# Optimization experiments

Measured on AMD Instinct MI355X. Metric: run time of the kernel, lower is better.

## Reference

```python
import jax, jax.numpy as jnp
import numpy as np

FM = 128       # feature_maps
QM = 128       # query_maps
ROUNDS = 4     # test_rounds (training=False)
N_VARS = 24576
N_CLAUSES = 98304
N_EDGES = 3 * N_CLAUSES
EPS = 1e-6


def _dense(k, fan_in, fan_out):
    return jax.random.normal(k, (fan_in, fan_out), jnp.float32) * (1.0 / np.sqrt(fan_in))


def setup_inputs() -> dict:
    key = jax.random.key(0)
    ks = jax.random.split(key, 20)
    return {
        "edge_lit": jax.random.randint(ks[0], (N_EDGES,), 0, 2 * N_VARS, dtype=jnp.int32),
        "edge_clause": jnp.sort(jax.random.randint(ks[1], (N_EDGES,), 0, N_CLAUSES, dtype=jnp.int32)),
        "noise_v": jax.random.normal(ks[2], (ROUNDS, N_VARS, 4), jnp.float32),
        "noise_c": jax.random.normal(ks[3], (ROUNDS, N_CLAUSES, 4), jnp.float32),
        # variables_query: MLP(2, QM, QM), input FM+4
        "vq_w0": _dense(ks[4], FM + 4, QM), "vq_b0": jnp.zeros((QM,), jnp.float32),
        "vq_w1": _dense(ks[5], QM, QM),     "vq_b1": jnp.zeros((QM,), jnp.float32),
        # clauses_query: MLP(2, QM, QM), input FM+4
        "cq_w0": _dense(ks[6], FM + 4, QM), "cq_b0": jnp.zeros((QM,), jnp.float32),
        "cq_w1": _dense(ks[7], QM, QM),     "cq_b1": jnp.zeros((QM,), jnp.float32),
        # clause_update: MLP(2, 2*FM, FM+QM), input FM+2*QM=384
        "cm_w0": _dense(ks[8], FM + 2 * QM, 2 * FM), "cm_b0": jnp.zeros((2 * FM,), jnp.float32),
        "cm_w1": _dense(ks[9], 2 * FM, FM + QM),     "cm_b1": jnp.zeros((FM + QM,), jnp.float32),
        # update_gate: MLP(3, 2*FM, FM), input QM+FM+2*QM=512
        "ug_w0": _dense(ks[10], QM + FM + 2 * QM, 2 * FM), "ug_b0": jnp.zeros((2 * FM,), jnp.float32),
        "ug_w1": _dense(ks[11], 2 * FM, 2 * FM),           "ug_b1": jnp.zeros((2 * FM,), jnp.float32),
        "ug_w2": _dense(ks[12], 2 * FM, FM),               "ug_b2": jnp.zeros((FM,), jnp.float32),
        # clauses_mask_output: MLP(2, FM, 1)
        "co_w0": _dense(ks[13], FM, FM), "co_b0": jnp.zeros((FM,), jnp.float32),
        "co_w1": _dense(ks[14], FM, 1),  "co_b1": jnp.zeros((1,), jnp.float32),
        "n_vars": N_VARS,
        "n_clauses": N_CLAUSES,
    }


def _forward(edge_lit, edge_clause, n_vars, n_clauses, floats):
    (noise_v, noise_c,
     vq_w0, vq_b0, vq_w1, vq_b1,
     cq_w0, cq_b0, cq_w1, cq_b1,
     cm_w0, cm_b0, cm_w1, cm_b1,
     ug_w0, ug_b0, ug_w1, ug_b1, ug_w2, ug_b2,
     co_w0, co_b0, co_w1, co_b1) = floats

    n_edges = edge_lit.shape[0]
    # lit_degree = row sums of sparse adjacency (all nonzeros are 1.0)
    lit_degree = jax.ops.segment_sum(jnp.ones((n_edges,), jnp.float32), edge_lit,
                                     num_segments=2 * n_vars)[:, None]          # [2V,1]
    degree_weight = jax.lax.rsqrt(jnp.maximum(lit_degree, 1.0))
    var_degree_weight = 4.0 * jax.lax.rsqrt(
        jnp.maximum(lit_degree[:n_vars] + lit_degree[n_vars:], 1.0))            # [V,1]

    def mlp2(x, w0, b0, w1, b1):
        return jax.nn.relu(x @ w0 + b0) @ w1 + b1

    def mlp3(x, w0, b0, w1, b1, w2, b2):
        h = jax.nn.relu(x @ w0 + b0)
        h = jax.nn.relu(h @ w1 + b1)
        return h @ w2 + b2

    def pair_norm(x):
        # PairNorm(subtract_mean=True), single graph -> global mean over nodes
        x = x - jnp.mean(x, axis=0, keepdims=True)
        return x * jax.lax.rsqrt(jnp.mean(jnp.square(x)) + EPS)

    def clauses_loss_fn(vq, cq):
        # unsat_cnf_clauses_loss: softplus literal values aggregated per clause,
        # clause satisfiability exp(-sum), gated by clause query mask.
        lits = jax.nn.softplus(jnp.concatenate([vq, -vq], axis=0))              # [2V,Q]
        csum = jax.ops.segment_sum(lits[edge_lit], edge_clause,
                                   num_segments=n_clauses)                      # [C,Q]
        loss = jnp.exp(-csum) * jax.nn.sigmoid(cq)
        return jnp.mean(loss), loss

    grad_fn = jax.grad(clauses_loss_fn, argnums=(0, 1), has_aux=True)

    def step(carry, xs):
        variables, clauses = carry
        nv, nc = xs
        vq = mlp2(jnp.concatenate([variables, nv], -1), vq_w0, vq_b0, vq_w1, vq_b1)
        cq = mlp2(jnp.concatenate([clauses, nc], -1), cq_w0, cq_b0, cq_w1, cq_b1)
        (vgrad, cgrad), clauses_loss = grad_fn(vq, cq)
        vgrad = vgrad * var_degree_weight
        clauses_loss = clauses_loss * 4.0
        clause_data = mlp2(jnp.concatenate([clauses, clauses_loss, cgrad], -1),
                           cm_w0, cm_b0, cm_w1, cm_b1)                          # [C,FM+QM]
        variables_loss_all = clause_data[:, :QM]
        clauses = pair_norm(clause_data[:, QM:]) * 0.25 + 0.1 * clauses
        # adj_matrix @ variables_loss_all (literal-side aggregation)
        variables_loss = jax.ops.segment_sum(variables_loss_all[edge_clause], edge_lit,
                                             num_segments=2 * n_vars) * degree_weight
        unit = jnp.concatenate([vgrad, variables,
                                variables_loss[:n_vars], variables_loss[n_vars:]], -1)
        variables = pair_norm(mlp3(unit, ug_w0, ug_b0, ug_w1, ug_b1, ug_w2, ug_b2)) * 0.25 \
                    + 0.1 * variables
        logits = mlp2(clauses, co_w0, co_b0, co_w1, co_b1)[:, 0]                # [C]
        return (variables, clauses), logits

    init = (jnp.ones((n_vars, FM), jnp.float32), jnp.ones((n_clauses, FM), jnp.float32))
    _, logits = jax.lax.scan(step, init, (noise_v, noise_c))                    # [R,C]
    return jax.nn.sigmoid(logits), jax.nn.softplus(logits)


def reference(edge_lit, edge_clause, noise_v, noise_c,
              vq_w0, vq_b0, vq_w1, vq_b1,
              cq_w0, cq_b0, cq_w1, cq_b1,
              cm_w0, cm_b0, cm_w1, cm_b1,
              ug_w0, ug_b0, ug_w1, ug_b1, ug_w2, ug_b2,
              co_w0, co_b0, co_w1, co_b1,
              n_vars, n_clauses):
    floats = (noise_v, noise_c,
              vq_w0, vq_b0, vq_w1, vq_b1,
              cq_w0, cq_b0, cq_w1, cq_b1,
              cm_w0, cm_b0, cm_w1, cm_b1,
              ug_w0, ug_b0, ug_w1, ug_b1, ug_w2, ug_b2,
              co_w0, co_b0, co_w1, co_b1)
    return _forward(edge_lit, edge_clause, int(n_vars), int(n_clauses), floats)
```

## Files before the change

### kernel.cpp

```cpp
#include <hip/hip_runtime.h>
#include <math.h>

#define NV 24576
#define NC 98304
#define NE 294912
#define CMCHUNK 24576

typedef unsigned short bf16;
typedef _Float16 f16;
using bf8 = __attribute__((ext_vector_type(8))) short;
using f4  = __attribute__((ext_vector_type(4))) float;

static constexpr float INV_CQM = 1.0f / 12582912.0f;
static constexpr float LOG2E = 1.44269504f;
static constexpr float LN2 = 0.69314718f;

__device__ __forceinline__ float b2f(bf16 h) { return __uint_as_float(((unsigned)h) << 16); }
__device__ __forceinline__ bf16 f2b(float f) {
  unsigned u = __float_as_uint(f);
  u += 0x7fff + ((u >> 16) & 1);
  return (bf16)(u >> 16);
}
__device__ __forceinline__ float fexp2(float x) { float r; asm("v_exp_f32 %0, %1" : "=v"(r) : "v"(x)); return r; }
__device__ __forceinline__ float flog2(float x) { float r; asm("v_log_f32 %0, %1" : "=v"(r) : "v"(x)); return r; }
__device__ __forceinline__ float frcpf(float x) { float r; asm("v_rcp_f32 %0, %1" : "=v"(r) : "v"(x)); return r; }
__device__ __forceinline__ float fsigm(float x) { return frcpf(1.0f + fexp2(-x * LOG2E)); }
__device__ __forceinline__ float fsoftplus(float x) {
  return fmaxf(x, 0.0f) + LN2 * flog2(1.0f + fexp2(-fabsf(x) * LOG2E));
}
__device__ __forceinline__ float cvt_ld(float x) { return x; }
__device__ __forceinline__ float cvt_ld(bf16 x) { return b2f(x); }

__device__ __forceinline__ void gload16(const void* g, void* l) {
  __builtin_amdgcn_global_load_lds((const __attribute__((address_space(1))) unsigned int*)g,
                                   (__attribute__((address_space(3))) unsigned int*)l, 16, 0, 0);
}


__global__ __launch_bounds__(256) void k_cptr(const int* __restrict__ ec, int* __restrict__ ptr) {
  int c = blockIdx.x * 256 + threadIdx.x;
  if (c > NC) return;
  int lo = 0, hi = NE;
  while (lo < hi) { int mid = (lo + hi) >> 1; if (ec[mid] < c) lo = mid + 1; else hi = mid; }
  ptr[c] = lo;
}

__global__ __launch_bounds__(256) void k_litcnt(const int* __restrict__ el, int* __restrict__ cnt) {
  int e = blockIdx.x * 256 + threadIdx.x;
  atomicAdd(&cnt[el[e]], 1);
}

__global__ __launch_bounds__(1024) void k_scan(int* __restrict__ cnt, int* __restrict__ ptr) {
  __shared__ int wsum[16];
  __shared__ int carry_s;
  int tid = threadIdx.x, lane = tid & 63, w = tid >> 6;
  if (tid == 0) carry_s = 0;
  __syncthreads();
  for (int base = 0; base < 2 * NV; base += 1024) {
    int x = cnt[base + tid];
    int v = x;
#pragma unroll
    for (int off = 1; off < 64; off <<= 1) {
      int y = __shfl_up(v, off, 64);
      if (lane >= off) v += y;
    }
    if (lane == 63) wsum[w] = v;
    __syncthreads();
    int carry = carry_s;
    int wpre = 0;
    for (int i = 0; i < w; ++i) wpre += wsum[i];
    int excl = carry + wpre + (v - x);
    ptr[base + tid] = excl;
    cnt[base + tid] = excl;
    __syncthreads();
    if (tid == 1023) carry_s = carry + wpre + v;
  }
  __syncthreads();
  if (tid == 0) ptr[2 * NV] = carry_s;
}

__global__ __launch_bounds__(256) void k_fillsort(const int* __restrict__ el, const int* __restrict__ ec,
                                                  int* __restrict__ cur, int* __restrict__ lclause) {
  int e = blockIdx.x * 256 + threadIdx.x;
  int pos = atomicAdd(&cur[el[e]], 1);
  lclause[pos] = ec[e];
}

__global__ __launch_bounds__(256) void k_degree(const int* __restrict__ lptr, float* __restrict__ dw,
                                                float* __restrict__ vdw) {
  int l = blockIdx.x * 256 + threadIdx.x;
  if (l < 2 * NV) dw[l] = rsqrtf(fmaxf((float)(lptr[l + 1] - lptr[l]), 1.0f));
  if (l < NV) {
    int d = (lptr[l + 1] - lptr[l]) + (lptr[l + NV + 1] - lptr[l + NV]);
    vdw[l] = 4.0f * rsqrtf(fmaxf((float)d, 1.0f));
  }
}

__global__ __launch_bounds__(256) void k_init_v(float* __restrict__ variables, bf16* __restrict__ ugA) {
  int i = blockIdx.x * 256 + threadIdx.x;
  variables[i] = 1.0f;
  ugA[(size_t)(i >> 7) * 512 + 128 + (i & 127)] = 0x3F80;
}
__global__ __launch_bounds__(256) void k_init_c(bf16* __restrict__ cmA) {
  int i = blockIdx.x * 256 + threadIdx.x;
  cmA[(size_t)(i >> 7) * 384 + (i & 127)] = 0x3F80;
}

__global__ __launch_bounds__(256) void k_wt(const float* __restrict__ w, bf16* __restrict__ wt,
                                            int K, int N, int Kpad) {
  int idx = blockIdx.x * 256 + threadIdx.x;
  int n = idx / Kpad, k = idx % Kpad;
  if (n >= N) return;
  wt[idx] = (k < K) ? f2b(w[(size_t)k * N + n]) : (bf16)0;
}


template <int KDIM, bool CONCAT, bool RELU, int OUT>
__global__ __launch_bounds__(256) void mgemm(const bf16* __restrict__ A0, int lda,
                                             const float* __restrict__ noise,
                                             const bf16* __restrict__ WT,
                                             const float* __restrict__ Bv,
                                             void* out0, void* out1, int ldOut) {
  __shared__ __align__(16) char smem[65536];
  constexpr int NT = KDIM / 64;
  const int tid = threadIdx.x;
  const int m0 = blockIdx.x * 128;
  const int n0 = blockIdx.y * 128;
  const int lane = tid & 63;
  const int w = tid >> 6;
  const int wr = w >> 1, wc = w & 1;
  const int rl = (tid >> 3) & 7;
  const int cc = tid & 7;
  const int swzoff = (cc * 16) ^ (rl << 4);

  auto stage = [&](int t, int buf) {
    char* As = smem + buf * 32768;
    char* Bs = As + 16384;
    const int k0 = t * 64;
    if (!CONCAT || k0 < 128) {
#pragma unroll
      for (int it = 0; it < 4; ++it) {
        int row0 = it * 32 + w * 8;
        int row = row0 + rl;
        gload16((const char*)(A0 + (size_t)(m0 + row) * lda + k0) + swzoff, As + row0 * 128);
        gload16((const char*)(WT + (size_t)(n0 + row) * KDIM + k0) + swzoff, Bs + row0 * 128);
      }
    } else {
      const int srow = tid >> 3, schunk = tid & 7;
#pragma unroll
      for (int it = 0; it < 4; ++it) {
        int row = srow + it * 32;
        alignas(16) bf16 tmp[8];
#pragma unroll
        for (int e = 0; e < 8; ++e) {
          int kk = schunk * 8 + e;
          tmp[e] = (kk < 4) ? f2b(noise[(size_t)(m0 + row) * 4 + kk]) : (bf16)0;
        }
        *reinterpret_cast<uint4*>(&As[row * 128 + ((schunk * 16) ^ ((row & 7) << 4))]) =
            *reinterpret_cast<uint4*>(tmp);
        int row0 = it * 32 + w * 8;
        gload16((const char*)(WT + (size_t)(n0 + row0 + rl) * KDIM + k0) + swzoff, Bs + row0 * 128);
      }
    }
  };

  f4 acc[4][4] = {};
  stage(0, 0);
#pragma unroll
  for (int t = 0; t < NT; ++t) {
    const int buf = t & 1;
    __builtin_amdgcn_sched_barrier(0);
    if (t + 1 < NT) {
      stage(t + 1, buf ^ 1);
      if (CONCAT && (t + 1) * 64 >= 128) {
        asm volatile("s_waitcnt vmcnt(4) lgkmcnt(0)" ::: "memory");
      } else {
        asm volatile("s_waitcnt vmcnt(8) lgkmcnt(0)" ::: "memory");
      }
    } else {
      asm volatile("s_waitcnt vmcnt(0) lgkmcnt(0)" ::: "memory");
    }
    __builtin_amdgcn_s_barrier();
    __builtin_amdgcn_sched_barrier(0);
    const char* As = smem + buf * 32768;
    const char* Bs = As + 16384;
#pragma unroll
    for (int kk = 0; kk < 2; ++kk) {
      bf8 a[4], b[4];
#pragma unroll
      for (int i = 0; i < 4; ++i) {
        int r = wr * 64 + i * 16 + (lane & 15);
        int cby = (kk * 64 + ((lane >> 4) * 16)) ^ ((r & 7) << 4);
        a[i] = *reinterpret_cast<const bf8*>(&As[r * 128 + cby]);
        int c = wc * 64 + i * 16 + (lane & 15);
        int cby2 = (kk * 64 + ((lane >> 4) * 16)) ^ ((c & 7) << 4);
        b[i] = *reinterpret_cast<const bf8*>(&Bs[c * 128 + cby2]);
      }
#pragma unroll
      for (int i = 0; i < 4; ++i)
#pragma unroll
        for (int j = 0; j < 4; ++j)
          acc[i][j] = __builtin_amdgcn_mfma_f32_16x16x32_bf16(a[i], b[j], acc[i][j], 0, 0, 0);
    }
    __builtin_amdgcn_sched_barrier(0);
    __builtin_amdgcn_s_barrier();
  }
  const int colloc = wc * 64 + (lane & 15);
  const int rowbase = m0 + wr * 64 + ((lane >> 4) << 2);

  if constexpr (OUT == 4) {
    const float* w1 = (const float*)out1;
    float* outp = (float*)out0;
    const int t = ldOut;
    float part[4][4];
#pragma unroll
    for (int i = 0; i < 4; ++i)
#pragma unroll
      for (int p = 0; p < 4; ++p) part[i][p] = 0.0f;
#pragma unroll
    for (int j = 0; j < 4; ++j) {
      int c = colloc + j * 16;
      float bias = Bv[c];
      float w1c = w1[c];
#pragma unroll
      for (int i = 0; i < 4; ++i)
#pragma unroll
        for (int p = 0; p < 4; ++p)
          part[i][p] += fmaxf(acc[i][j][p] + bias, 0.0f) * w1c;
    }
#pragma unroll
    for (int m = 1; m < 16; m <<= 1)
#pragma unroll
      for (int i = 0; i < 4; ++i)
#pragma unroll
        for (int p = 0; p < 4; ++p)
          part[i][p] += __shfl_xor(part[i][p], m, 64);
    float* red = (float*)smem;
    if ((lane & 15) == 0) {
#pragma unroll
      for (int i = 0; i < 4; ++i)
#pragma unroll
        for (int p = 0; p < 4; ++p)
          red[wc * 128 + wr * 64 + i * 16 + ((lane >> 4) << 2) + p] = part[i][p];
    }
    __syncthreads();
    if (tid < 128) {
      float lg = red[tid] + red[128 + tid] + noise[0];
      int row = m0 + tid;
      outp[(size_t)t * NC + row] = fsigm(lg);
      outp[(size_t)4 * NC + (size_t)t * NC + row] = fsoftplus(lg);
    }
    return;
  }

#pragma unroll
  for (int j = 0; j < 4; ++j) {
    int c = n0 + colloc + j * 16;
    float bias = Bv[c];
#pragma unroll
    for (int i = 0; i < 4; ++i) {
      int rb = rowbase + i * 16;
#pragma unroll
      for (int p = 0; p < 4; ++p) {
        float v = acc[i][j][p] + bias;
        if (RELU) v = fmaxf(v, 0.0f);
        int r = rb + p;
        if constexpr (OUT == 0) {
          ((float*)out0)[(size_t)r * ldOut + c] = v;
        } else if constexpr (OUT == 1) {
          ((bf16*)out0)[(size_t)r * ldOut + c] = f2b(v);
        } else if constexpr (OUT == 2) {
          bf16* o = (c < 128) ? (bf16*)out0 : (bf16*)out1;
          o[(size_t)r * 128 + (c & 127)] = f2b(v);
        } else {
          float tq = LN2 * flog2(1.0f + fexp2(-fabsf(v) * LOG2E));
          ((f16*)out0)[(size_t)r * 128 + c] = (f16)(fmaxf(v, 0.0f) + tq);
          ((f16*)out1)[(size_t)r * 128 + c] = (f16)(fmaxf(-v, 0.0f) + tq);
        }
      }
    }
  }
}


__global__ __launch_bounds__(256) void k_loss(const int* __restrict__ edge_lit, const int* __restrict__ cptr,
                                              const f16* __restrict__ sp, const bf16* __restrict__ cq,
                                              bf16* __restrict__ cmA) {
  const int g = threadIdx.x >> 7;
  const int q = threadIdx.x & 127;
  const int c0 = blockIdx.x * 16 + g * 8;
#pragma unroll
  for (int ci = 0; ci < 8; ++ci) {
    int c = c0 + ci;
    int e0 = cptr[c], e1 = cptr[c + 1];
    float csum = 0.0f;
    for (int e = e0; e < e1; e += 4) {
#pragma unroll
      for (int k = 0; k < 4; ++k) {
        int ee = e + k;
        bool ok = ee < e1;
        int lit = ok ? edge_lit[ee] : 0;
        float v = ok ? (float)sp[(size_t)lit * 128 + q] : 0.0f;
        csum += v;
      }
    }
    float s = fsigm(b2f(cq[(size_t)c * 128 + q]));
    float L = fexp2(-csum * LOG2E) * s;
    cmA[(size_t)c * 384 + 128 + q] = f2b(4.0f * L);
    cmA[(size_t)c * 384 + 256 + q] = f2b(L * (1.0f - s) * INV_CQM);
  }
}

__global__ __launch_bounds__(256) void k_gatherv(const int* __restrict__ lptr, const int* __restrict__ lclause,
                                                 const bf16* __restrict__ cmA, const bf16* __restrict__ cd0,
                                                 const f16* __restrict__ spn, const float* __restrict__ dw,
                                                 const float* __restrict__ vdw, bf16* __restrict__ ugA) {
  int v = blockIdx.x;
  int half = threadIdx.x >> 7, q = threadIdx.x & 127;
  int l = v + half * NV;
  int j0 = lptr[l], j1 = lptr[l + 1];
  float sg = 0.0f, sv = 0.0f;
  for (int j = j0; j < j1; j += 4) {
#pragma unroll
    for (int k = 0; k < 4; ++k) {
      int jj = j + k;
      bool ok = jj < j1;
      int c = ok ? lclause[jj] : 0;
      float a = ok ? b2f(cmA[(size_t)c * 384 + 128 + q]) : 0.0f;
      float b = ok ? b2f(cd0[(size_t)c * 128 + q]) : 0.0f;
      sg += a;
      sv += b;
    }
  }
  __shared__ float sgl[2][128];
  sgl[half][q] = sg;
  ugA[(size_t)v * 512 + 256 + half * 128 + q] = f2b(sv * dw[l]);
  __syncthreads();
  if (half == 0) {
    float s = fexp2(-LOG2E * (float)spn[(size_t)v * 128 + q]);
    float g = ((1.0f - s) * sgl[1][q] - s * sgl[0][q]) * (INV_CQM * 0.25f) * vdw[v];
    ugA[(size_t)v * 512 + q] = f2b(g);
  }
}

template <typename T>
__global__ __launch_bounds__(256) void k_pn_stats(const T* __restrict__ X, int R, float* __restrict__ stats) {
  int q = threadIdx.x & 127;
  int rg = threadIdx.x >> 7;
  float cs = 0.0f, ss = 0.0f;
  for (int r = blockIdx.x * 2 + rg; r < R; r += gridDim.x * 2) {
    float x = cvt_ld(X[(size_t)r * 128 + q]);
    cs += x;
    ss += x * x;
  }
  __shared__ float scs[256], sss[256];
  scs[threadIdx.x] = cs;
  sss[threadIdx.x] = ss;
  __syncthreads();
  if (threadIdx.x < 128) atomicAdd(&stats[q], scs[q] + scs[128 + q]);
  for (int off = 128; off; off >>= 1) {
    if (threadIdx.x < off) sss[threadIdx.x] += sss[threadIdx.x + off];
    __syncthreads();
  }
  if (threadIdx.x == 0) atomicAdd(&stats[128], sss[0]);
}

__global__ __launch_bounds__(128) void k_pn_final(float* __restrict__ stats, float R) {
  __shared__ float s[128];
  int q = threadIdx.x;
  float m = stats[q] / R;
  s[q] = m * m;
  __syncthreads();
  for (int off = 64; off; off >>= 1) {
    if (q < off) s[q] += s[q + off];
    __syncthreads();
  }
  if (q == 0) {
    float var = (stats[128] - R * s[0]) / (R * 128.0f);
    stats[129] = rsqrtf(fmaxf(var, 0.0f) + 1e-6f) * 0.25f;
  }
  stats[q] = m;
}

__global__ __launch_bounds__(256) void k_pn_apply_c(const bf16* __restrict__ cd1, const float* __restrict__ stats,
                                                    bf16* __restrict__ cmA) {
  int i = blockIdx.x * 256 + threadIdx.x;
  int c = i >> 7, q = i & 127;
  float x = b2f(cd1[i]);
  float old = b2f(cmA[(size_t)c * 384 + q]);
  cmA[(size_t)c * 384 + q] = f2b((x - stats[q]) * stats[129] + 0.1f * old);
}

__global__ __launch_bounds__(256) void k_pn_apply_v(const float* __restrict__ uout, const float* __restrict__ stats,
                                                    float* __restrict__ variables, bf16* __restrict__ ugA) {
  int i = blockIdx.x * 256 + threadIdx.x;
  int v = i >> 7, q = i & 127;
  float nv = (uout[i] - stats[q]) * stats[129] + 0.1f * variables[i];
  variables[i] = nv;
  ugA[(size_t)v * 512 + 128 + q] = f2b(nv);
}


extern "C" void kernel_launch(void* const* d_in, const int* in_sizes, int n_in,
                              void* d_out, int out_size, void* d_ws, size_t ws_size,
                              hipStream_t stream) {
  const int* edge_lit = (const int*)d_in[0];
  const int* edge_clause = (const int*)d_in[1];
  const float* noise_v = (const float*)d_in[2];
  const float* noise_c = (const float*)d_in[3];
  const float* vq_w0 = (const float*)d_in[4];  const float* vq_b0 = (const float*)d_in[5];
  const float* vq_w1 = (const float*)d_in[6];  const float* vq_b1 = (const float*)d_in[7];
  const float* cq_w0 = (const float*)d_in[8];  const float* cq_b0 = (const float*)d_in[9];
  const float* cq_w1 = (const float*)d_in[10]; const float* cq_b1 = (const float*)d_in[11];
  const float* cm_w0 = (const float*)d_in[12]; const float* cm_b0 = (const float*)d_in[13];
  const float* cm_w1 = (const float*)d_in[14]; const float* cm_b1 = (const float*)d_in[15];
  const float* ug_w0 = (const float*)d_in[16]; const float* ug_b0 = (const float*)d_in[17];
  const float* ug_w1 = (const float*)d_in[18]; const float* ug_b1 = (const float*)d_in[19];
  const float* ug_w2 = (const float*)d_in[20]; const float* ug_b2 = (const float*)d_in[21];
  const float* co_w0 = (const float*)d_in[22]; const float* co_b0 = (const float*)d_in[23];
  const float* co_w1 = (const float*)d_in[24]; const float* co_b1 = (const float*)d_in[25];
  float* out = (float*)d_out;

  char* base = (char*)d_ws;
  size_t off = 0;
  auto A = [&](size_t n) -> char* {
    char* p = base + off;
    off = (off + n + 255) & ~(size_t)255;
    return p;
  };
  float* variables = (float*)A((size_t)NV * 128 * 4);
  bf16* cmA        = (bf16*)A((size_t)NC * 384 * 2);
  bf16* ugA        = (bf16*)A((size_t)NV * 512 * 2);
  char* R_cq       = A((size_t)NC * 128 * 2);
  char* R_h        = A((size_t)NC * 128 * 2);
  char* R_big      = A((size_t)2 * NV * 128 * 2 + (size_t)NV * 128 * 4);
  bf16* wtb        = (bf16*)A(983424);
  int* cptr = (int*)A((size_t)(NC + 1) * 4);
  int* lptr = (int*)A((size_t)(2 * NV + 1) * 4);
  int* lcur = (int*)A((size_t)2 * NV * 4);
  int* lclause = (int*)A((size_t)NE * 4);
  float* dw  = (float*)A((size_t)2 * NV * 4);
  float* vdw = (float*)A((size_t)NV * 4);
  float* stats = (float*)A(2048);
  if (off > ws_size) {
    hipMemsetAsync(d_out, 0xFF, (size_t)out_size * 4, stream);
    return;
  }

  bf16* cq  = (bf16*)R_cq;
  bf16* cd0 = (bf16*)R_cq;
  bf16* hv  = (bf16*)R_h;
  bf16* hc  = (bf16*)R_h;
  bf16* cd1 = (bf16*)R_h;
  bf16* uh1 = (bf16*)R_h;
  bf16* uh2 = (bf16*)(R_h + (size_t)NV * 256 * 2);
  bf16* cmh = (bf16*)R_big;
  f16* spp  = (f16*)(R_big + 12582912);
  f16* spn  = spp + (size_t)NV * 128;
  float* uout = (float*)(R_big + 12582912);

  size_t wo = 0;
  auto WTa = [&](int n, int kp) { bf16* p = wtb + wo; wo += (size_t)n * kp; return p; };
  bf16* wt_vq0 = WTa(128, 192); bf16* wt_vq1 = WTa(128, 128);
  bf16* wt_cq0 = WTa(128, 192); bf16* wt_cq1 = WTa(128, 128);
  bf16* wt_cm0 = WTa(256, 384); bf16* wt_cm1 = WTa(256, 256);
  bf16* wt_ug0 = WTa(256, 512); bf16* wt_ug1 = WTa(256, 256);
  bf16* wt_ug2 = WTa(128, 256); bf16* wt_co0 = WTa(128, 128);

  hipMemsetAsync(lcur, 0, (size_t)2 * NV * 4, stream);
  k_cptr<<<(NC + 256) / 256, 256, 0, stream>>>(edge_clause, cptr);
  k_litcnt<<<NE / 256, 256, 0, stream>>>(edge_lit, lcur);
  k_scan<<<1, 1024, 0, stream>>>(lcur, lptr);
  k_fillsort<<<NE / 256, 256, 0, stream>>>(edge_lit, edge_clause, lcur, lclause);
  k_degree<<<(2 * NV + 255) / 256, 256, 0, stream>>>(lptr, dw, vdw);
  k_init_v<<<NV * 128 / 256, 256, 0, stream>>>(variables, ugA);
  k_init_c<<<NC * 128 / 256, 256, 0, stream>>>(cmA);
  k_wt<<<128 * 192 / 256, 256, 0, stream>>>(vq_w0, wt_vq0, 132, 128, 192);
  k_wt<<<128 * 128 / 256, 256, 0, stream>>>(vq_w1, wt_vq1, 128, 128, 128);
  k_wt<<<128 * 192 / 256, 256, 0, stream>>>(cq_w0, wt_cq0, 132, 128, 192);
  k_wt<<<128 * 128 / 256, 256, 0, stream>>>(cq_w1, wt_cq1, 128, 128, 128);
  k_wt<<<256 * 384 / 256, 256, 0, stream>>>(cm_w0, wt_cm0, 384, 256, 384);
  k_wt<<<256 * 256 / 256, 256, 0, stream>>>(cm_w1, wt_cm1, 256, 256, 256);
  k_wt<<<256 * 512 / 256, 256, 0, stream>>>(ug_w0, wt_ug0, 512, 256, 512);
  k_wt<<<256 * 256 / 256, 256, 0, stream>>>(ug_w1, wt_ug1, 256, 256, 256);
  k_wt<<<128 * 256 / 256, 256, 0, stream>>>(ug_w2, wt_ug2, 256, 128, 256);
  k_wt<<<128 * 128 / 256, 256, 0, stream>>>(co_w0, wt_co0, 128, 128, 128);

  for (int t = 0; t < 4; ++t) {
    const float* nvp = noise_v + (size_t)t * NV * 4;
    const float* ncp = noise_c + (size_t)t * NC * 4;
    mgemm<192, true, true, 1><<<dim3(NV / 128, 1), 256, 0, stream>>>(ugA + 128, 512, nvp, wt_vq0, vq_b0, hv, nullptr, 128);
    mgemm<128, false, false, 3><<<dim3(NV / 128, 1), 256, 0, stream>>>(hv, 128, nullptr, wt_vq1, vq_b1, spp, spn, 128);
    mgemm<192, true, true, 1><<<dim3(NC / 128, 1), 256, 0, stream>>>(cmA, 384, ncp, wt_cq0, cq_b0, hc, nullptr, 128);
    mgemm<128, false, false, 1><<<dim3(NC / 128, 1), 256, 0, stream>>>(hc, 128, nullptr, wt_cq1, cq_b1, cq, nullptr, 128);
    k_loss<<<NC / 16, 256, 0, stream>>>(edge_lit, cptr, spp, cq, cmA);
    for (int ch = 0; ch < NC / CMCHUNK; ++ch) {
      size_t ro = (size_t)ch * CMCHUNK;
      mgemm<384, false, true, 1><<<dim3(CMCHUNK / 128, 2), 256, 0, stream>>>(cmA + ro * 384, 384, nullptr, wt_cm0, cm_b0, cmh, nullptr, 256);
      mgemm<256, false, false, 2><<<dim3(CMCHUNK / 128, 2), 256, 0, stream>>>(cmh, 256, nullptr, wt_cm1, cm_b1, cd0 + ro * 128, cd1 + ro * 128, 128);
    }
    k_gatherv<<<NV, 256, 0, stream>>>(lptr, lclause, cmA, cd0, spn, dw, vdw, ugA);
    hipMemsetAsync(stats, 0, 132 * 4, stream);
    k_pn_stats<bf16><<<256, 256, 0, stream>>>(cd1, NC, stats);
    k_pn_final<<<1, 128, 0, stream>>>(stats, (float)NC);
    k_pn_apply_c<<<NC * 128 / 256, 256, 0, stream>>>(cd1, stats, cmA);
    mgemm<128, false, false, 4><<<dim3(NC / 128, 1), 256, 0, stream>>>(cmA, 384, co_b1, wt_co0, co_b0, out, (void*)co_w1, t);
    mgemm<512, false, true, 1><<<dim3(NV / 128, 2), 256, 0, stream>>>(ugA, 512, nullptr, wt_ug0, ug_b0, uh1, nullptr, 256);
    mgemm<256, false, true, 1><<<dim3(NV / 128, 2), 256, 0, stream>>>(uh1, 256, nullptr, wt_ug1, ug_b1, uh2, nullptr, 256);
    mgemm<256, false, false, 0><<<dim3(NV / 128, 1), 256, 0, stream>>>(uh2, 256, nullptr, wt_ug2, ug_b2, uout, nullptr, 128);
    hipMemsetAsync(stats, 0, 132 * 4, stream);
    k_pn_stats<float><<<256, 256, 0, stream>>>(uout, NV, stats);
    k_pn_final<<<1, 128, 0, stream>>>(stats, (float)NV);
    k_pn_apply_v<<<NV * 128 / 256, 256, 0, stream>>>(uout, stats, variables, ugA);
  }
}
```

Before: 1.940 ms.

## Merge variable and clause query GEMMs into dual launches and compact clause buffers

Pairs the variable-query and clause-query MLP layers into a single launch each, so one grid covers both problems and the launch count drops. The clause feature buffer shrinks from 384 to 256 columns, and a separate gbuf holds the loss term and cd0 interleaved. The clause-update GEMM now reads its A operand from two buffers, and the gather kernel reads both values from one contiguous row. This is meant to reduce launch overhead, fill the GPU better on the small GEMMs, and improve gather locality, at the cost of more complex operand addressing.

```diff
diff --git a/kernel.cpp b/kernel.cpp
--- a/kernel.cpp
+++ b/kernel.cpp
@@ -103,7 +103,7 @@
 }
 __global__ __launch_bounds__(256) void k_init_c(bf16* __restrict__ cmA) {
   int i = blockIdx.x * 256 + threadIdx.x;
-  cmA[(size_t)(i >> 7) * 384 + (i & 127)] = 0x3F80;
+  cmA[(size_t)(i >> 7) * 256 + (i & 127)] = 0x3F80;
 }
 
 __global__ __launch_bounds__(256) void k_wt(const float* __restrict__ w, bf16* __restrict__ wt,
@@ -115,16 +115,19 @@
 }
 
 
-template <int KDIM, bool CONCAT, bool RELU, int OUT>
-__global__ __launch_bounds__(256) void mgemm(const bf16* __restrict__ A0, int lda,
-                                             const float* __restrict__ noise,
-                                             const bf16* __restrict__ WT,
-                                             const float* __restrict__ Bv,
-                                             void* out0, void* out1, int ldOut) {
-  __shared__ __align__(16) char smem[65536];
+struct GP {
+  const bf16* A0; const bf16* A1; int lda;
+  const float* noise; const bf16* WT; const float* Bv;
+  void* o0; void* o1; int ldOut;
+};
+
+enum { AL_STD = 0, AL_NOISE = 1, AL_CM = 2 };
+
+template <int KDIM, int AL, bool RELU, int OUT>
+__device__ __forceinline__ void gemm_body(const GP g, int bx, char* smem) {
   constexpr int NT = KDIM / 64;
   const int tid = threadIdx.x;
-  const int m0 = blockIdx.x * 128;
+  const int m0 = bx * 128;
   const int n0 = blockIdx.y * 128;
   const int lane = tid & 63;
   const int w = tid >> 6;
@@ -137,15 +140,7 @@
     char* As = smem + buf * 32768;
     char* Bs = As + 16384;
     const int k0 = t * 64;
-    if (!CONCAT || k0 < 128) {
-#pragma unroll
-      for (int it = 0; it < 4; ++it) {
-        int row0 = it * 32 + w * 8;
-        int row = row0 + rl;
-        gload16((const char*)(A0 + (size_t)(m0 + row) * lda + k0) + swzoff, As + row0 * 128);
-        gload16((const char*)(WT + (size_t)(n0 + row) * KDIM + k0) + swzoff, Bs + row0 * 128);
-      }
-    } else {
+    if (AL == AL_NOISE && t == 2) {
       const int srow = tid >> 3, schunk = tid & 7;
 #pragma unroll
       for (int it = 0; it < 4; ++it) {
@@ -154,12 +149,26 @@
 #pragma unroll
         for (int e = 0; e < 8; ++e) {
           int kk = schunk * 8 + e;
-          tmp[e] = (kk < 4) ? f2b(noise[(size_t)(m0 + row) * 4 + kk]) : (bf16)0;
+          tmp[e] = (kk < 4) ? f2b(g.noise[(size_t)(m0 + row) * 4 + kk]) : (bf16)0;
         }
         *reinterpret_cast<uint4*>(&As[row * 128 + ((schunk * 16) ^ ((row & 7) << 4))]) =
             *reinterpret_cast<uint4*>(tmp);
         int row0 = it * 32 + w * 8;
-        gload16((const char*)(WT + (size_t)(n0 + row0 + rl) * KDIM + k0) + swzoff, Bs + row0 * 128);
+        gload16((const char*)(g.WT + (size_t)(n0 + row0 + rl) * KDIM + k0) + swzoff, Bs + row0 * 128);
+      }
+    } else {
+      const bf16* Ap = g.A0;
+      int co_ = k0;
+      if (AL == AL_CM) {
+        if (t >= 2 && t < 4) Ap = g.A1;
+        if (t >= 2) co_ = k0 - 128;
+      }
+#pragma unroll
+      for (int it = 0; it < 4; ++it) {
+        int row0 = it * 32 + w * 8;
+        int row = row0 + rl;
+        gload16((const char*)(Ap + (size_t)(m0 + row) * g.lda + co_) + swzoff, As + row0 * 128);
+        gload16((const char*)(g.WT + (size_t)(n0 + row) * KDIM + k0) + swzoff, Bs + row0 * 128);
       }
     }
   };
@@ -172,7 +181,7 @@
     __builtin_amdgcn_sched_barrier(0);
     if (t + 1 < NT) {
       stage(t + 1, buf ^ 1);
-      if (CONCAT && (t + 1) * 64 >= 128) {
+      if (AL == AL_NOISE && t + 1 == 2) {
         asm volatile("s_waitcnt vmcnt(4) lgkmcnt(0)" ::: "memory");
       } else {
         asm volatile("s_waitcnt vmcnt(8) lgkmcnt(0)" ::: "memory");
@@ -209,9 +218,9 @@
   const int rowbase = m0 + wr * 64 + ((lane >> 4) << 2);
 
   if constexpr (OUT == 4) {
-    const float* w1 = (const float*)out1;
-    float* outp = (float*)out0;
-    const int t = ldOut;
+    const float* w1 = (const float*)g.o1;
+    float* outp = (float*)g.o0;
+    const int t = g.ldOut;
     float part[4][4];
 #pragma unroll
     for (int i = 0; i < 4; ++i)
@@ -220,7 +229,7 @@
 #pragma unroll
     for (int j = 0; j < 4; ++j) {
       int c = colloc + j * 16;
-      float bias = Bv[c];
+      float bias = g.Bv[c];
       float w1c = w1[c];
 #pragma unroll
       for (int i = 0; i < 4; ++i)
@@ -245,7 +254,7 @@
     }
     __syncthreads();
     if (tid < 128) {
-      float lg = red[tid] + red[128 + tid] + noise[0];
+      float lg = red[tid] + red[128 + tid] + g.noise[0];
       int row = m0 + tid;
       outp[(size_t)t * NC + row] = fsigm(lg);
       outp[(size_t)4 * NC + (size_t)t * NC + row] = fsoftplus(lg);
@@ -256,7 +265,7 @@
 #pragma unroll
   for (int j = 0; j < 4; ++j) {
     int c = n0 + colloc + j * 16;
-    float bias = Bv[c];
+    float bias = g.Bv[c];
 #pragma unroll
     for (int i = 0; i < 4; ++i) {
       int rb = rowbase + i * 16;
@@ -266,25 +275,38 @@
         if (RELU) v = fmaxf(v, 0.0f);
         int r = rb + p;
         if constexpr (OUT == 0) {
-          ((float*)out0)[(size_t)r * ldOut + c] = v;
+          ((float*)g.o0)[(size_t)r * g.ldOut + c] = v;
         } else if constexpr (OUT == 1) {
-          ((bf16*)out0)[(size_t)r * ldOut + c] = f2b(v);
+          ((bf16*)g.o0)[(size_t)r * g.ldOut + c] = f2b(v);
         } else if constexpr (OUT == 2) {
-          bf16* o = (c < 128) ? (bf16*)out0 : (bf16*)out1;
-          o[(size_t)r * 128 + (c & 127)] = f2b(v);
+          if (c < 128) ((bf16*)g.o0)[(size_t)r * 256 + c] = f2b(v);
+          else ((bf16*)g.o1)[(size_t)r * 128 + (c - 128)] = f2b(v);
         } else {
           float tq = LN2 * flog2(1.0f + fexp2(-fabsf(v) * LOG2E));
-          ((f16*)out0)[(size_t)r * 128 + c] = (f16)(fmaxf(v, 0.0f) + tq);
-          ((f16*)out1)[(size_t)r * 128 + c] = (f16)(fmaxf(-v, 0.0f) + tq);
+          ((f16*)g.o0)[(size_t)r * 128 + c] = (f16)(fmaxf(v, 0.0f) + tq);
+          ((f16*)g.o1)[(size_t)r * 128 + c] = (f16)(fmaxf(-v, 0.0f) + tq);
         }
       }
     }
   }
 }
 
+template <int KDIM, int AL, bool RELU, int OUT>
+__global__ __launch_bounds__(256) void mgemm_s(GP g) {
+  __shared__ __align__(16) char smem[65536];
+  gemm_body<KDIM, AL, RELU, OUT>(g, blockIdx.x, smem);
+}
+
+template <int KDIM, int AL, bool RELU, int OUTA, int OUTB>
+__global__ __launch_bounds__(256) void mgemm_d(GP ga, GP gb, int nA) {
+  __shared__ __align__(16) char smem[65536];
+  if ((int)blockIdx.x < nA) gemm_body<KDIM, AL, RELU, OUTA>(ga, blockIdx.x, smem);
+  else gemm_body<KDIM, AL, RELU, OUTB>(gb, blockIdx.x - nA, smem);
+}
+
 
 __global__ __launch_bounds__(256) void k_loss(const int* __restrict__ edge_lit, const int* __restrict__ cptr,
-                                              const f16* __restrict__ sp, const bf16* __restrict__ cq,
+                                              const f16* __restrict__ sp, bf16* __restrict__ gbuf,
                                               bf16* __restrict__ cmA) {
   const int g = threadIdx.x >> 7;
   const int q = threadIdx.x & 127;
@@ -304,17 +326,17 @@
         csum += v;
       }
     }
-    float s = fsigm(b2f(cq[(size_t)c * 128 + q]));
+    float s = fsigm(b2f(gbuf[(size_t)c * 256 + 128 + q]));
     float L = fexp2(-csum * LOG2E) * s;
-    cmA[(size_t)c * 384 + 128 + q] = f2b(4.0f * L);
-    cmA[(size_t)c * 384 + 256 + q] = f2b(L * (1.0f - s) * INV_CQM);
+    gbuf[(size_t)c * 256 + q] = f2b(4.0f * L);
+    cmA[(size_t)c * 256 + 128 + q] = f2b(L * (1.0f - s) * INV_CQM);
   }
 }
 
 __global__ __launch_bounds__(256) void k_gatherv(const int* __restrict__ lptr, const int* __restrict__ lclause,
-                                                 const bf16* __restrict__ cmA, const bf16* __restrict__ cd0,
-                                                 const f16* __restrict__ spn, const float* __restrict__ dw,
-                                                 const float* __restrict__ vdw, bf16* __restrict__ ugA) {
+                                                 const bf16* __restrict__ gbuf, const f16* __restrict__ spn,
+                                                 const float* __restrict__ dw, const float* __restrict__ vdw,
+                                                 bf16* __restrict__ ugA) {
   int v = blockIdx.x;
   int half = threadIdx.x >> 7, q = threadIdx.x & 127;
   int l = v + half * NV;
@@ -326,8 +348,8 @@
       int jj = j + k;
       bool ok = jj < j1;
       int c = ok ? lclause[jj] : 0;
-      float a = ok ? b2f(cmA[(size_t)c * 384 + 128 + q]) : 0.0f;
-      float b = ok ? b2f(cd0[(size_t)c * 128 + q]) : 0.0f;
+      float a = ok ? b2f(gbuf[(size_t)c * 256 + q]) : 0.0f;
+      float b = ok ? b2f(gbuf[(size_t)c * 256 + 128 + q]) : 0.0f;
       sg += a;
       sv += b;
     }
@@ -387,8 +409,8 @@
   int i = blockIdx.x * 256 + threadIdx.x;
   int c = i >> 7, q = i & 127;
   float x = b2f(cd1[i]);
-  float old = b2f(cmA[(size_t)c * 384 + q]);
-  cmA[(size_t)c * 384 + q] = f2b((x - stats[q]) * stats[129] + 0.1f * old);
+  float old = b2f(cmA[(size_t)c * 256 + q]);
+  cmA[(size_t)c * 256 + q] = f2b((x - stats[q]) * stats[129] + 0.1f * old);
 }
 
 __global__ __launch_bounds__(256) void k_pn_apply_v(const float* __restrict__ uout, const float* __restrict__ stats,
@@ -429,9 +451,9 @@
     return p;
   };
   float* variables = (float*)A((size_t)NV * 128 * 4);
-  bf16* cmA        = (bf16*)A((size_t)NC * 384 * 2);
+  bf16* cmA        = (bf16*)A((size_t)NC * 256 * 2);
+  bf16* gbuf       = (bf16*)A((size_t)NC * 256 * 2);
   bf16* ugA        = (bf16*)A((size_t)NV * 512 * 2);
-  char* R_cq       = A((size_t)NC * 128 * 2);
   char* R_h        = A((size_t)NC * 128 * 2);
   char* R_big      = A((size_t)2 * NV * 128 * 2 + (size_t)NV * 128 * 4);
   bf16* wtb        = (bf16*)A(983424);
@@ -447,13 +469,11 @@
     return;
   }
 
-  bf16* cq  = (bf16*)R_cq;
-  bf16* cd0 = (bf16*)R_cq;
-  bf16* hv  = (bf16*)R_h;
   bf16* hc  = (bf16*)R_h;
   bf16* cd1 = (bf16*)R_h;
   bf16* uh1 = (bf16*)R_h;
   bf16* uh2 = (bf16*)(R_h + (size_t)NV * 256 * 2);
+  bf16* hv  = (bf16*)R_big;
   bf16* cmh = (bf16*)R_big;
   f16* spp  = (f16*)(R_big + 12582912);
   f16* spn  = spp + (size_t)NV * 128;
@@ -489,25 +509,45 @@
   for (int t = 0; t < 4; ++t) {
     const float* nvp = noise_v + (size_t)t * NV * 4;
     const float* ncp = noise_c + (size_t)t * NC * 4;
-    mgemm<192, true, true, 1><<<dim3(NV / 128, 1), 256, 0, stream>>>(ugA + 128, 512, nvp, wt_vq0, vq_b0, hv, nullptr, 128);
-    mgemm<128, false, false, 3><<<dim3(NV / 128, 1), 256, 0, stream>>>(hv, 128, nullptr, wt_vq1, vq_b1, spp, spn, 128);
-    mgemm<192, true, true, 1><<<dim3(NC / 128, 1), 256, 0, stream>>>(cmA, 384, ncp, wt_cq0, cq_b0, hc, nullptr, 128);
-    mgemm<128, false, false, 1><<<dim3(NC / 128, 1), 256, 0, stream>>>(hc, 128, nullptr, wt_cq1, cq_b1, cq, nullptr, 128);
-    k_loss<<<NC / 16, 256, 0, stream>>>(edge_lit, cptr, spp, cq, cmA);
+    {
+      GP pa{ugA + 128, nullptr, 512, nvp, wt_vq0, vq_b0, hv, nullptr, 128};
+      GP pb{cmA, nullptr, 256, ncp, wt_cq0, cq_b0, hc, nullptr, 128};
+      mgemm_d<192, AL_NOISE, true, 1, 1><<<dim3(960, 1), 256, 0, stream>>>(pa, pb, 192);
+    }
+    {
+      GP pa{hv, nullptr, 128, nullptr, wt_vq1, vq_b1, spp, spn, 128};
+      GP pb{hc, nullptr, 128, nullptr, wt_cq1, cq_b1, gbuf + 128, nullptr, 256};
+      mgemm_d<128, AL_STD, false, 3, 1><<<dim3(960, 1), 256, 0, stream>>>(pa, pb, 192);
+    }
+    k_loss<<<NC / 16, 256, 0, stream>>>(edge_lit, cptr, spp, gbuf, cmA);
     for (int ch = 0; ch < NC / CMCHUNK; ++ch) {
       size_t ro = (size_t)ch * CMCHUNK;
-      mgemm<384, false, true, 1><<<dim3(CMCHUNK / 128, 2), 256, 0, stream>>>(cmA + ro * 384, 384, nullptr, wt_cm0, cm_b0, cmh, nullptr, 256);
-      mgemm<256, false, false, 2><<<dim3(CMCHUNK / 128, 2), 256, 0, stream>>>(cmh, 256, nullptr, wt_cm1, cm_b1, cd0 + ro * 128, cd1 + ro * 128, 128);
-    }
-    k_gatherv<<<NV, 256, 0, stream>>>(lptr, lclause, cmA, cd0, spn, dw, vdw, ugA);
+      GP p0{cmA + ro * 256, gbuf + ro * 256, 256, nullptr, wt_cm0, cm_b0, cmh, nullptr, 256};
+      mgemm_s<384, AL_CM, true, 1><<<dim3(CMCHUNK / 128, 2), 256, 0, stream>>>(p0);
+      GP p1{cmh, nullptr, 256, nullptr, wt_cm1, cm_b1, gbuf + ro * 256 + 128, cd1 + ro * 128, 0};
+      mgemm_s<256, AL_STD, false, 2><<<dim3(CMCHUNK / 128, 2), 256, 0, stream>>>(p1);
+    }
+    k_gatherv<<<NV, 256, 0, stream>>>(lptr, lclause, gbuf, spn, dw, vdw, ugA);
     hipMemsetAsync(stats, 0, 132 * 4, stream);
     k_pn_stats<bf16><<<256, 256, 0, stream>>>(cd1, NC, stats);
     k_pn_final<<<1, 128, 0, stream>>>(stats, (float)NC);
     k_pn_apply_c<<<NC * 128 / 256, 256, 0, stream>>>(cd1, stats, cmA);
-    mgemm<128, false, false, 4><<<dim3(NC / 128, 1), 256, 0, stream>>>(cmA, 384, co_b1, wt_co0, co_b0, out, (void*)co_w1, t);
-    mgemm<512, false, true, 1><<<dim3(NV / 128, 2), 256, 0, stream>>>(ugA, 512, nullptr, wt_ug0, ug_b0, uh1, nullptr, 256);
-    mgemm<256, false, true, 1><<<dim3(NV / 128, 2), 256, 0, stream>>>(uh1, 256, nullptr, wt_ug1, ug_b1, uh2, nullptr, 256);
-    mgemm<256, false, false, 0><<<dim3(NV / 128, 1), 256, 0, stream>>>(uh2, 256, nullptr, wt_ug2, ug_b2, uout, nullptr, 128);
+    {
+      GP p{cmA, nullptr, 256, co_b1, wt_co0, co_b0, out, (void*)co_w1, t};
+      mgemm_s<128, AL_STD, false, 4><<<dim3(NC / 128, 1), 256, 0, stream>>>(p);
+    }
+    {
+      GP p{ugA, nullptr, 512, nullptr, wt_ug0, ug_b0, uh1, nullptr, 256};
+      mgemm_s<512, AL_STD, true, 1><<<dim3(NV / 128, 2), 256, 0, stream>>>(p);
+    }
+    {
+      GP p{uh1, nullptr, 256, nullptr, wt_ug1, ug_b1, uh2, nullptr, 256};
+      mgemm_s<256, AL_STD, true, 1><<<dim3(NV / 128, 2), 256, 0, stream>>>(p);
+    }
+    {
+      GP p{uh2, nullptr, 256, nullptr, wt_ug2, ug_b2, uout, nullptr, 128};
+      mgemm_s<256, AL_STD, false, 0><<<dim3(NV / 128, 1), 256, 0, stream>>>(p);
+    }
     hipMemsetAsync(stats, 0, 132 * 4, stream);
     k_pn_stats<float><<<256, 256, 0, stream>>>(uout, NV, stats);
     k_pn_final<<<1, 128, 0, stream>>>(stats, (float)NV);
```

New measurement: 1.903 ms. No clear change (-1.9%).
